# Optimization experiments

Hardware: AMD Instinct MI355X
Metric: run time of the kernel (lower is better)

The kernel has to match this reference:

```python
import jax, jax.numpy as jnp
import numpy as np

N, D, DP, H, S = 768, 384, 128, 8, 32
EPS = 1e-5  # haiku LayerNorm default eps


def _ln(x):
    # hk.LayerNorm([-1], create_scale=False, create_offset=False)
    mu = jnp.mean(x, axis=-1, keepdims=True)
    var = jnp.var(x, axis=-1, keepdims=True)
    return (x - mu) * jax.lax.rsqrt(var + EPS)


def setup_inputs() -> dict:
    key = jax.random.key(0)
    ks = jax.random.split(key, 12)
    local = jax.random.normal(ks[0], (N, D), dtype=jnp.float32)
    pair = jax.random.normal(ks[1], (N, N, DP), dtype=jnp.float32)
    mask = jnp.ones((N,), dtype=bool)
    sc = 0.02
    Wq = jax.random.normal(ks[2], (D, H * S), jnp.float32) * sc
    bq = jnp.zeros((H * S,), jnp.float32)
    Wk = jax.random.normal(ks[3], (D, H * S), jnp.float32) * sc
    bk = jnp.zeros((H * S,), jnp.float32)
    Wv = jax.random.normal(ks[4], (D, H * S), jnp.float32) * sc
    bv = jnp.zeros((H * S,), jnp.float32)
    Wpb = jax.random.normal(ks[5], (DP, H), jnp.float32) * sc   # pair -> attn bias, no bias term
    Wpv = jax.random.normal(ks[6], (DP, S), jnp.float32) * sc   # pair -> pair value, no bias term
    Wo = jax.random.normal(ks[7], (2 * H * S, D), jnp.float32) * sc  # zeros-init in original; random for testing
    return dict(local=local, pair=pair, mask=mask, Wq=Wq, bq=bq, Wk=Wk, bk=bk,
                Wv=Wv, bv=bv, Wpb=Wpb, Wpv=Wpv, Wo=Wo)


def reference(local, pair, mask, Wq, bq, Wk, bk, Wv, bv, Wpb, Wpv, Wo):
    n = local.shape[0]
    local_n = _ln(local)                       # [N, D]
    pair_n = _ln(pair)                         # [N, N, DP]

    q = _ln((local_n @ Wq + bq).reshape(n, H, S)) * (1.0 / jnp.sqrt(S + 1e-6))
    k = _ln((local_n @ Wk + bk).reshape(n, H, S))
    v = (local_n @ Wv + bv).reshape(n, H, S)

    pair_mask = mask[:, None] & mask[None, :]  # [N, N]
    attn = jnp.einsum('iha,jha->ijh', q, k)    # [N, N, H]
    attn = attn + jnp.einsum('ijd,dh->ijh', pair_n, Wpb)
    attn = jnp.where(pair_mask[..., None], attn, -1e9)
    attn = jax.nn.softmax(attn, axis=1)
    attn = jnp.where(pair_mask[..., None], attn, 0.0)

    out = jnp.einsum('ijh,jha->iha', attn, v).reshape(n, H * S)
    out_pair = jnp.einsum('ijd,da->ija', pair_n, Wpv)           # [N, N, S]
    out_pair = jnp.einsum('ijh,ija->iha', attn, out_pair).reshape(n, H * S)
    out = jnp.concatenate((out, out_pair), axis=-1)             # [N, 2*H*S]
    return out @ Wo                                             # [N, D]
```

## Files before the change

kernel.cpp:

```cpp
#include <hip/hip_runtime.h>

#define Nn 768
#define Dd 384
#define DPp 128
#define Hh 8
#define Ss 32

typedef short bf16x8 __attribute__((ext_vector_type(8)));
typedef float f32x4 __attribute__((ext_vector_type(4)));

__device__ __forceinline__ unsigned short f2bf(float f) {
  unsigned int u = __float_as_uint(f);
  u += 0x7fffu + ((u >> 16) & 1u);
  return (unsigned short)(u >> 16);
}
__device__ __forceinline__ float bf2f(unsigned short b) {
  return __uint_as_float(((unsigned int)b) << 16);
}

__global__ void k_prep(const float* __restrict__ Wpb, const float* __restrict__ Wpv,
                       const float* __restrict__ Wo,
                       unsigned short* __restrict__ wt, unsigned short* __restrict__ wot) {
  if (blockIdx.x < 12) {
    int idx = blockIdx.x * 512 + threadIdx.x;
    int o = idx >> 7, d = idx & 127;
    float v = 0.f;
    if (o < 8)       v = Wpb[d * 8 + o];
    else if (o < 40) v = Wpv[d * 32 + (o - 8)];
    wt[idx] = f2bf(v);
  } else {
    int n = blockIdx.x - 12;
    int k = threadIdx.x;
    wot[n * 512 + k] = f2bf(Wo[k * 384 + n]);
  }
}

__global__ __launch_bounds__(256)
void k_qkv(const float* __restrict__ local,
           const float* __restrict__ Wq, const float* __restrict__ bq,
           const float* __restrict__ Wk, const float* __restrict__ bk,
           const float* __restrict__ Wv, const float* __restrict__ bv,
           float* __restrict__ qw, float* __restrict__ kw, float* __restrict__ vw,
           unsigned short* __restrict__ vt, unsigned short* __restrict__ kt) {
  const int t = threadIdx.x;
  const int i0 = blockIdx.x * 4;
  __shared__ float xn[4][384];
  __shared__ float red[4][4][2];

  float a0[4], a1[4];
#pragma unroll
  for (int r = 0; r < 4; ++r) {
    const float* xr = local + (size_t)(i0 + r) * 384;
    a0[r] = xr[t];
    a1[r] = (t < 128) ? xr[256 + t] : 0.f;
    float s = a0[r] + a1[r];
    float s2 = a0[r] * a0[r] + a1[r] * a1[r];
#pragma unroll
    for (int m = 1; m < 64; m <<= 1) { s += __shfl_xor(s, m); s2 += __shfl_xor(s2, m); }
    if ((t & 63) == 0) { red[r][t >> 6][0] = s; red[r][t >> 6][1] = s2; }
  }
  __syncthreads();
#pragma unroll
  for (int r = 0; r < 4; ++r) {
    float s  = red[r][0][0] + red[r][1][0] + red[r][2][0] + red[r][3][0];
    float s2 = red[r][0][1] + red[r][1][1] + red[r][2][1] + red[r][3][1];
    float mu = s * (1.f / 384.f);
    float rr = rsqrtf(s2 * (1.f / 384.f) - mu * mu + 1e-5f);
    xn[r][t] = (a0[r] - mu) * rr;
    if (t < 128) xn[r][256 + t] = (a1[r] - mu) * rr;
  }
  __syncthreads();

  float accq[4], acck[4], accv[4];
  const float bqv = bq[t], bkv = bk[t], bvv = bv[t];
#pragma unroll
  for (int r = 0; r < 4; ++r) { accq[r] = bqv; acck[r] = bkv; accv[r] = bvv; }

  for (int dq = 0; dq < 96; ++dq) {
    float4 xv[4];
#pragma unroll
    for (int r = 0; r < 4; ++r) xv[r] = ((const float4*)xn[r])[dq];
#pragma unroll
    for (int e = 0; e < 4; ++e) {
      const int d = dq * 4 + e;
      const float wqv = Wq[d * 256 + t];
      const float wkv = Wk[d * 256 + t];
      const float wvv = Wv[d * 256 + t];
#pragma unroll
      for (int r = 0; r < 4; ++r) {
        float xe = (e == 0) ? xv[r].x : (e == 1) ? xv[r].y : (e == 2) ? xv[r].z : xv[r].w;
        accq[r] += xe * wqv; acck[r] += xe * wkv; accv[r] += xe * wvv;
      }
    }
  }

#pragma unroll
  for (int r = 0; r < 4; ++r) {
    float qs = accq[r], qs2 = accq[r] * accq[r];
    float ks = acck[r], ks2 = acck[r] * acck[r];
#pragma unroll
    for (int m = 1; m < 32; m <<= 1) {
      qs += __shfl_xor(qs, m); qs2 += __shfl_xor(qs2, m);
      ks += __shfl_xor(ks, m); ks2 += __shfl_xor(ks2, m);
    }
    float qmu = qs * (1.f / 32.f);
    float qr = rsqrtf(qs2 * (1.f / 32.f) - qmu * qmu + 1e-5f);
    float kmu = ks * (1.f / 32.f);
    float kr = rsqrtf(ks2 * (1.f / 32.f) - kmu * kmu + 1e-5f);
    size_t o = (size_t)(i0 + r) * 256 + t;
    float qv = (accq[r] - qmu) * qr * 0.17677669f;
    float kv = (acck[r] - kmu) * kr;
    qw[o] = qv;
    kw[o] = kv;
    vw[o] = accv[r];
    kt[o] = f2bf(kv);
    vt[(size_t)t * 768 + (i0 + r)] = f2bf(accv[r]);
  }
}

__global__ __launch_bounds__(256)
void k_pairA(const float* __restrict__ pair, const unsigned short* __restrict__ wt,
             unsigned short* __restrict__ biasb, unsigned short* __restrict__ pvg) {
  const int b = blockIdx.x;
  const int i = b / 12, jt = b % 12;
  const int j0 = jt * 64;
  const int tid = threadIdx.x;
  const int lane = tid & 63, w = tid >> 6;

  __shared__ unsigned short A_s[64 * 136];
  __shared__ unsigned short Wt_s[48 * 136];
  __shared__ float2 mur_s[64];

  for (int idx = tid; idx < 1536; idx += 256) {
    int row = idx >> 5, c = idx & 31;
    *(uint2*)(Wt_s + row * 136 + c * 4) = ((const uint2*)wt)[idx];
  }

  const float4* src = (const float4*)(pair + ((size_t)i * 768 + j0) * 128);
  float4 x[8];
#pragma unroll
  for (int u = 0; u < 8; ++u) x[u] = src[u * 256 + tid];

  const int half = lane >> 5;
#pragma unroll
  for (int u = 0; u < 8; ++u) {
    float4 v = x[u];
    float sm = v.x + v.y + v.z + v.w;
    float s2 = v.x * v.x + v.y * v.y + v.z * v.z + v.w * v.w;
    sm += __shfl_xor(sm, 1);  s2 += __shfl_xor(s2, 1);
    sm += __shfl_xor(sm, 2);  s2 += __shfl_xor(s2, 2);
    sm += __shfl_xor(sm, 4);  s2 += __shfl_xor(s2, 4);
    sm += __shfl_xor(sm, 8);  s2 += __shfl_xor(s2, 8);
    sm += __shfl_xor(sm, 16); s2 += __shfl_xor(s2, 16);
    if ((lane & 31) == 0) {
      float mu = sm * (1.f / 128.f);
      float rr = rsqrtf(s2 * (1.f / 128.f) - mu * mu + 1e-5f);
      mur_s[u * 8 + w * 2 + half] = make_float2(mu, rr);
    }
  }
  __syncthreads();

#pragma unroll
  for (int u = 0; u < 8; ++u) {
    int row = u * 8 + (tid >> 5);
    int c4 = tid & 31;
    float2 mr = mur_s[row];
    float4 v = x[u];
    unsigned int lo = ((unsigned int)f2bf((v.y - mr.x) * mr.y) << 16) | f2bf((v.x - mr.x) * mr.y);
    unsigned int hi = ((unsigned int)f2bf((v.w - mr.x) * mr.y) << 16) | f2bf((v.z - mr.x) * mr.y);
    *(uint2*)(A_s + row * 136 + c4 * 4) = make_uint2(lo, hi);
  }
  __syncthreads();

  const int col = lane & 15, q4 = lane >> 4;
  f32x4 acc0 = {0.f, 0.f, 0.f, 0.f}, acc1 = acc0, acc2 = acc0;
#pragma unroll
  for (int kk = 0; kk < 4; ++kk) {
    bf16x8 af = *(const bf16x8*)(A_s + (w * 16 + col) * 136 + kk * 32 + q4 * 8);
    bf16x8 b0 = *(const bf16x8*)(Wt_s + (col)      * 136 + kk * 32 + q4 * 8);
    bf16x8 b1 = *(const bf16x8*)(Wt_s + (16 + col) * 136 + kk * 32 + q4 * 8);
    bf16x8 b2 = *(const bf16x8*)(Wt_s + (32 + col) * 136 + kk * 32 + q4 * 8);
    acc0 = __builtin_amdgcn_mfma_f32_16x16x32_bf16(af, b0, acc0, 0, 0, 0);
    acc1 = __builtin_amdgcn_mfma_f32_16x16x32_bf16(af, b1, acc1, 0, 0, 0);
    acc2 = __builtin_amdgcn_mfma_f32_16x16x32_bf16(af, b2, acc2, 0, 0, 0);
  }
  __syncthreads();

  unsigned short* pv_st = A_s;
  unsigned short* b_st  = A_s + 2112;
  const int jl = w * 16 + q4 * 4;
#pragma unroll
  for (int reg = 0; reg < 4; ++reg) {
    int j = jl + reg;
    pv_st[j * 33 + (col + 8)] = f2bf(acc1[reg]);
    if (col < 8) {
      b_st[j * 9 + col] = f2bf(acc0[reg]);
      pv_st[j * 33 + (col + 24)] = f2bf(acc2[reg]);
    } else {
      pv_st[j * 33 + (col - 8)] = f2bf(acc0[reg]);
    }
  }
  __syncthreads();

  {
    const int a = tid >> 3, jc = tid & 7;
    unsigned short buf[8];
#pragma unroll
    for (int r = 0; r < 8; ++r) buf[r] = pv_st[(jc * 8 + r) * 33 + a];
    *(uint4*)(pvg + ((size_t)i * 32 + a) * 768 + j0 + jc * 8) = *(uint4*)buf;
  }
  if (tid < 64) {
    const int h = tid >> 3, jc = tid & 7;
    unsigned short buf[8];
#pragma unroll
    for (int r = 0; r < 8; ++r) buf[r] = b_st[(jc * 8 + r) * 9 + h];
    *(uint4*)(biasb + ((size_t)i * 8 + h) * 768 + j0 + jc * 8) = *(uint4*)buf;
  }
}

__device__ __forceinline__ float dot8(uint4 r, float4 qa, float4 qb) {
  return bf2f((unsigned short)(r.x & 0xffffu)) * qa.x + bf2f((unsigned short)(r.x >> 16)) * qa.y
       + bf2f((unsigned short)(r.y & 0xffffu)) * qa.z + bf2f((unsigned short)(r.y >> 16)) * qa.w
       + bf2f((unsigned short)(r.z & 0xffffu)) * qb.x + bf2f((unsigned short)(r.z >> 16)) * qb.y
       + bf2f((unsigned short)(r.w & 0xffffu)) * qb.z + bf2f((unsigned short)(r.w >> 16)) * qb.w;
}

__global__ __launch_bounds__(512)
void k_soft(const unsigned short* __restrict__ biasb,
            const float* __restrict__ qw, const unsigned short* __restrict__ kt,
            unsigned short* __restrict__ pbuf) {
  const int i = blockIdx.x;
  const int tid = threadIdx.x;
  const int lane = tid & 63;
  const int wv = tid >> 6;

  __shared__ float logit_s[8 * 776];
  __shared__ float q_s[256];

  const unsigned short* bsrc = biasb + (size_t)i * 6144;
  for (int idx = tid; idx < 1536; idx += 512) {
    uint2 w = ((const uint2*)bsrc)[idx];
    int h = idx / 192, c = (idx % 192) * 4;
    float* dst = logit_s + h * 776 + c;
    dst[0] = bf2f((unsigned short)(w.x & 0xffffu));
    dst[1] = bf2f((unsigned short)(w.x >> 16));
    dst[2] = bf2f((unsigned short)(w.y & 0xffffu));
    dst[3] = bf2f((unsigned short)(w.y >> 16));
  }
  if (tid < 256) q_s[tid] = qw[(size_t)i * 256 + tid];
  __syncthreads();

  for (int rep = 0; rep < 12; ++rep) {
    int idx = rep * 512 + tid;
    int j = idx >> 3, h = idx & 7;
    const unsigned short* kp = kt + (size_t)j * 256 + h * 32;
    const float4* qp = (const float4*)(q_s + h * 32);
    uint4 r0 = *(const uint4*)(kp);
    uint4 r1 = *(const uint4*)(kp + 8);
    uint4 r2 = *(const uint4*)(kp + 16);
    uint4 r3 = *(const uint4*)(kp + 24);
    float d = dot8(r0, qp[0], qp[1]) + dot8(r1, qp[2], qp[3])
            + dot8(r2, qp[4], qp[5]) + dot8(r3, qp[6], qp[7]);
    logit_s[h * 776 + j] += d;
  }
  __syncthreads();

  {
    const int h = wv;
    float* lr = logit_s + h * 776;
    float mx = -3.0e38f;
#pragma unroll
    for (int rr = 0; rr < 12; ++rr) mx = fmaxf(mx, lr[rr * 64 + lane]);
#pragma unroll
    for (int m = 1; m < 64; m <<= 1) mx = fmaxf(mx, __shfl_xor(mx, m));
    float e[12];
    float sum = 0.f;
#pragma unroll
    for (int rr = 0; rr < 12; ++rr) {
      e[rr] = __expf(lr[rr * 64 + lane] - mx);
      sum += e[rr];
    }
#pragma unroll
    for (int m = 1; m < 64; m <<= 1) sum += __shfl_xor(sum, m);
    const float rinv = 1.f / sum;
    unsigned short* dst = pbuf + ((size_t)h * 768 + i) * 768;
#pragma unroll
    for (int rr = 0; rr < 12; ++rr)
      dst[rr * 64 + lane] = f2bf(e[rr] * rinv);
  }
}

__global__ __launch_bounds__(128)
void k_mm(const unsigned short* __restrict__ pbuf, const unsigned short* __restrict__ vt,
          const unsigned short* __restrict__ pvg, unsigned short* __restrict__ concat_bf) {
  const int b = blockIdx.x;
  const int tid = threadIdx.x;
  const int nt = tid >> 6, lane = tid & 63;
  const int col = lane & 15, q4 = lane >> 4;

  if (b < 384) {
    const int h = b / 48, it = b % 48;
    const int i0 = it * 16;
    const unsigned short* ap = pbuf + ((size_t)h * 768 + i0 + col) * 768 + q4 * 8;
    const unsigned short* bp = vt + ((size_t)h * 32 + nt * 16 + col) * 768 + q4 * 8;
    f32x4 acc = {0.f, 0.f, 0.f, 0.f};
#pragma unroll
    for (int kk = 0; kk < 24; ++kk) {
      bf16x8 a = *(const bf16x8*)(ap + kk * 32);
      bf16x8 bb = *(const bf16x8*)(bp + kk * 32);
      acc = __builtin_amdgcn_mfma_f32_16x16x32_bf16(a, bb, acc, 0, 0, 0);
    }
#pragma unroll
    for (int reg = 0; reg < 4; ++reg) {
      int i = i0 + q4 * 4 + reg;
      concat_bf[(size_t)i * 512 + h * 32 + nt * 16 + col] = f2bf(acc[reg]);
    }
  } else {
    const int i = b - 384;
    const int hrow = (col < 8) ? col : 7;
    const unsigned short* ap = pbuf + ((size_t)hrow * 768 + i) * 768 + q4 * 8;
    const unsigned short* bp = pvg + ((size_t)i * 32 + nt * 16 + col) * 768 + q4 * 8;
    f32x4 acc = {0.f, 0.f, 0.f, 0.f};
#pragma unroll
    for (int kk = 0; kk < 24; ++kk) {
      bf16x8 a = *(const bf16x8*)(ap + kk * 32);
      bf16x8 bb = *(const bf16x8*)(bp + kk * 32);
      acc = __builtin_amdgcn_mfma_f32_16x16x32_bf16(a, bb, acc, 0, 0, 0);
    }
    if (q4 < 2) {
#pragma unroll
      for (int reg = 0; reg < 4; ++reg) {
        int hh = q4 * 4 + reg;
        concat_bf[(size_t)i * 512 + 256 + hh * 32 + nt * 16 + col] = f2bf(acc[reg]);
      }
    }
  }
}

__global__ __launch_bounds__(256)
void k_out2(const unsigned short* __restrict__ concat_bf, const unsigned short* __restrict__ wot,
            float* __restrict__ out) {
  const int b = blockIdx.x;
  const int i0 = (b / 6) * 16;
  const int tid = threadIdx.x;
  const int nt = tid >> 6, lane = tid & 63;
  const int n0 = (b % 6) * 64 + nt * 16;
  const int col = lane & 15, q4 = lane >> 4;

  const unsigned short* ap = concat_bf + (size_t)(i0 + col) * 512 + q4 * 8;
  const unsigned short* bp = wot + (size_t)(n0 + col) * 512 + q4 * 8;
  f32x4 acc = {0.f, 0.f, 0.f, 0.f};
#pragma unroll
  for (int kk = 0; kk < 16; ++kk) {
    bf16x8 a = *(const bf16x8*)(ap + kk * 32);
    bf16x8 bb = *(const bf16x8*)(bp + kk * 32);
    acc = __builtin_amdgcn_mfma_f32_16x16x32_bf16(a, bb, acc, 0, 0, 0);
  }
#pragma unroll
  for (int reg = 0; reg < 4; ++reg) {
    int i = i0 + q4 * 4 + reg;
    out[(size_t)i * 384 + n0 + col] = acc[reg];
  }
}

__global__ __launch_bounds__(512)
void k_pair_fused(const float* __restrict__ pair,
                  const float* __restrict__ qw, const float* __restrict__ kw,
                  const float* __restrict__ vw, const unsigned short* __restrict__ wt,
                  float* __restrict__ concat) {
  const int i = blockIdx.x;
  const int tid = threadIdx.x;
  const int lane = tid & 63;
  const int wv = tid >> 6;

  __shared__ float xt[64 * 132];
  __shared__ unsigned short A_s[64 * 136];
  __shared__ unsigned short Wt_s[48 * 136];
  __shared__ unsigned short pv_s[32 * 772];
  __shared__ float logit_s[768 * 9];
  __shared__ float2 mur_s[64];
  __shared__ float q_s[256];
  __shared__ float rinv_s[8];

  for (int idx = tid; idx < 48 * 128; idx += 512)
    Wt_s[(idx >> 7) * 136 + (idx & 127)] = wt[idx];
  if (tid < 256) q_s[tid] = qw[(size_t)i * 256 + tid];

  for (int tt = 0; tt < 12; ++tt) {
    const int j0 = tt * 64;
    const float4* src = (const float4*)(pair + ((size_t)i * 768 + j0) * 128);
    __syncthreads();
#pragma unroll
    for (int r = 0; r < 4; ++r) {
      int qi = r * 512 + tid;
      float4 x = src[qi];
      ((float4*)(xt + (qi >> 5) * 132))[qi & 31] = x;
    }
    __syncthreads();
    if (tid < 256) {
      int j = tid >> 2, s = tid & 3;
      const float4* b = (const float4*)(xt + j * 132 + s * 32);
      float sm = 0.f, s2 = 0.f;
#pragma unroll
      for (int u = 0; u < 8; ++u) {
        float4 x = b[u];
        sm += x.x + x.y + x.z + x.w;
        s2 += x.x * x.x + x.y * x.y + x.z * x.z + x.w * x.w;
      }
      sm += __shfl_xor(sm, 1); s2 += __shfl_xor(s2, 1);
      sm += __shfl_xor(sm, 2); s2 += __shfl_xor(s2, 2);
      if (s == 0) {
        float mu = sm * (1.f / 128.f);
        float rr = rsqrtf(s2 * (1.f / 128.f) - mu * mu + 1e-5f);
        mur_s[j] = make_float2(mu, rr);
      }
    }
    __syncthreads();
#pragma unroll
    for (int r = 0; r < 4; ++r) {
      int qi = r * 512 + tid;
      int jj = qi >> 5, ql = qi & 31;
      float4 x = ((const float4*)(xt + jj * 132))[ql];
      float2 mr = mur_s[jj];
      unsigned int b01 = ((unsigned int)f2bf((x.y - mr.x) * mr.y) << 16) | f2bf((x.x - mr.x) * mr.y);
      unsigned int b23 = ((unsigned int)f2bf((x.w - mr.x) * mr.y) << 16) | f2bf((x.z - mr.x) * mr.y);
      *(uint2*)(A_s + jj * 136 + ql * 4) = make_uint2(b01, b23);
    }
    __syncthreads();
    if (wv < 4) {
      const int col = lane & 15, q4 = lane >> 4;
      f32x4 acc0 = {0.f, 0.f, 0.f, 0.f}, acc1 = acc0, acc2 = acc0;
#pragma unroll
      for (int kk = 0; kk < 4; ++kk) {
        bf16x8 af = *(const bf16x8*)(A_s + (wv * 16 + col) * 136 + kk * 32 + q4 * 8);
        bf16x8 b0 = *(const bf16x8*)(Wt_s + (col)      * 136 + kk * 32 + q4 * 8);
        bf16x8 b1 = *(const bf16x8*)(Wt_s + (16 + col) * 136 + kk * 32 + q4 * 8);
        bf16x8 b2 = *(const bf16x8*)(Wt_s + (32 + col) * 136 + kk * 32 + q4 * 8);
        acc0 = __builtin_amdgcn_mfma_f32_16x16x32_bf16(af, b0, acc0, 0, 0, 0);
        acc1 = __builtin_amdgcn_mfma_f32_16x16x32_bf16(af, b1, acc1, 0, 0, 0);
        acc2 = __builtin_amdgcn_mfma_f32_16x16x32_bf16(af, b2, acc2, 0, 0, 0);
      }
      const int jb = j0 + wv * 16 + q4 * 4;
#pragma unroll
      for (int reg = 0; reg < 4; ++reg) {
        int j = jb + reg;
        if (col < 8) logit_s[j * 9 + col] = acc0[reg];
        else         pv_s[(col - 8) * 772 + j] = f2bf(acc0[reg]);
        pv_s[(col + 8) * 772 + j] = f2bf(acc1[reg]);
        if (col < 8) pv_s[(col + 24) * 772 + j] = f2bf(acc2[reg]);
      }
    }
  }
  __syncthreads();

  for (int rep = 0; rep < 12; ++rep) {
    int idx = rep * 512 + tid;
    int j = idx >> 3, h = idx & 7;
    const float4* kp = (const float4*)(kw + ((size_t)j * 8 + h) * 32);
    const float4* qp = (const float4*)(q_s + h * 32);
    float d = 0.f;
#pragma unroll
    for (int u = 0; u < 8; ++u) {
      float4 a = qp[u], b = kp[u];
      d += a.x * b.x + a.y * b.y + a.z * b.z + a.w * b.w;
    }
    logit_s[j * 9 + h] += d;
  }
  __syncthreads();

  float* pT = xt;
  {
    const int h = wv;
    float mx = -3.0e38f;
#pragma unroll
    for (int rr = 0; rr < 12; ++rr) mx = fmaxf(mx, logit_s[(rr * 64 + lane) * 9 + h]);
#pragma unroll
    for (int m = 1; m < 64; m <<= 1) mx = fmaxf(mx, __shfl_xor(mx, m));
    float sum = 0.f;
#pragma unroll
    for (int rr = 0; rr < 12; ++rr) {
      int j = rr * 64 + lane;
      float e = __expf(logit_s[j * 9 + h] - mx);
      pT[h * 768 + j] = e;
      sum += e;
    }
#pragma unroll
    for (int m = 1; m < 64; m <<= 1) sum += __shfl_xor(sum, m);
    if (lane == 0) rinv_s[h] = 1.f / sum;
  }
  __syncthreads();

  float acc = 0.f;
  if (tid < 256) {
    const int h = tid >> 5, a = tid & 31;
    const float* vcol = vw + h * 32 + a;
    const float4* p4p = (const float4*)(pT + h * 768);
#pragma unroll 4
    for (int j4 = 0; j4 < 192; ++j4) {
      float4 p = p4p[j4];
      const float* vb = vcol + (size_t)(j4 * 4) * 256;
      acc += p.x * vb[0] + p.y * vb[256] + p.z * vb[512] + p.w * vb[768];
    }
    acc *= rinv_s[h];
  } else {
    const int u = tid - 256;
    const int h = u >> 5, a = u & 31;
    const float4* p4p = (const float4*)(pT + h * 768);
    const unsigned short* pvrow = pv_s + a * 772;
#pragma unroll 4
    for (int j4 = 0; j4 < 192; ++j4) {
      float4 p = p4p[j4];
      uint2 raw = *(const uint2*)(pvrow + j4 * 4);
      acc += p.x * bf2f((unsigned short)(raw.x & 0xffffu))
           + p.y * bf2f((unsigned short)(raw.x >> 16))
           + p.z * bf2f((unsigned short)(raw.y & 0xffffu))
           + p.w * bf2f((unsigned short)(raw.y >> 16));
    }
    acc *= rinv_s[h];
  }
  concat[(size_t)i * 512 + tid] = acc;
}

__global__ __launch_bounds__(384)
void k_out_f32(const float* __restrict__ concat, const float* __restrict__ Wo,
               float* __restrict__ out) {
  __shared__ float A_s[4 * 512];
  const int d = threadIdx.x;
  const int r0 = blockIdx.x * 4;
  const float4* src = (const float4*)(concat + (size_t)r0 * 512);
  for (int idx = d; idx < 512; idx += 384) ((float4*)A_s)[idx] = src[idx];
  __syncthreads();

  float acc[4] = {0.f, 0.f, 0.f, 0.f};
#pragma unroll 4
  for (int c4 = 0; c4 < 128; ++c4) {
    float w0 = Wo[(c4 * 4 + 0) * 384 + d];
    float w1 = Wo[(c4 * 4 + 1) * 384 + d];
    float w2 = Wo[(c4 * 4 + 2) * 384 + d];
    float w3 = Wo[(c4 * 4 + 3) * 384 + d];
#pragma unroll
    for (int r = 0; r < 4; ++r) {
      float4 a = ((const float4*)(A_s + r * 512))[c4];
      acc[r] += a.x * w0 + a.y * w1 + a.z * w2 + a.w * w3;
    }
  }
#pragma unroll
  for (int r = 0; r < 4; ++r) out[(size_t)(r0 + r) * 384 + d] = acc[r];
}

extern "C" void kernel_launch(void* const* d_in, const int* in_sizes, int n_in,
                              void* d_out, int out_size, void* d_ws, size_t ws_size,
                              hipStream_t stream) {
  (void)in_sizes; (void)n_in; (void)out_size;
  const float* local = (const float*)d_in[0];
  const float* pair  = (const float*)d_in[1];
  const float* Wq  = (const float*)d_in[3];
  const float* bq  = (const float*)d_in[4];
  const float* Wk  = (const float*)d_in[5];
  const float* bk  = (const float*)d_in[6];
  const float* Wv  = (const float*)d_in[7];
  const float* bv  = (const float*)d_in[8];
  const float* Wpb = (const float*)d_in[9];
  const float* Wpv = (const float*)d_in[10];
  const float* Wo  = (const float*)d_in[11];

  float* ws = (float*)d_ws;
  float* qw = ws;
  float* kw = qw + 196608;
  float* vw = kw + 196608;
  float* concat = vw + 196608;
  unsigned short* wt   = (unsigned short*)(concat + 393216);
  unsigned short* vt   = wt + 6144;
  unsigned short* kt   = vt + 196608;
  unsigned short* wot  = kt + 196608;
  unsigned short* biasb = wot + 196608;
  unsigned short* pvg  = biasb + 4718592;
  unsigned short* pbuf = pvg + 18874368;
  unsigned short* concat_bf = pbuf + 4718592;

  hipLaunchKernelGGL(k_prep, dim3(396), dim3(512), 0, stream, Wpb, Wpv, Wo, wt, wot);
  hipLaunchKernelGGL(k_qkv, dim3(192), dim3(256), 0, stream,
                     local, Wq, bq, Wk, bk, Wv, bv, qw, kw, vw, vt, kt);
  if (ws_size >= 62533632ull) {
    hipLaunchKernelGGL(k_pairA, dim3(9216), dim3(256), 0, stream, pair, wt, biasb, pvg);
    hipLaunchKernelGGL(k_soft, dim3(768), dim3(512), 0, stream, biasb, qw, kt, pbuf);
    hipLaunchKernelGGL(k_mm, dim3(1152), dim3(128), 0, stream, pbuf, vt, pvg, concat_bf);
    hipLaunchKernelGGL(k_out2, dim3(288), dim3(256), 0, stream, concat_bf, wot, (float*)d_out);
  } else {
    hipLaunchKernelGGL(k_pair_fused, dim3(768), dim3(512), 0, stream,
                       pair, qw, kw, vw, wt, concat);
    hipLaunchKernelGGL(k_out_f32, dim3(192), dim3(384), 0, stream, concat, Wo, (float*)d_out);
  }
}
```

Before: 537.7 us.

## Fuse QK logits into pair kernel and merge prep with QKV kernel

The q·k dot products move out of the softmax kernel into the pair-projection kernel. There they are added in fp32 to the pair bias before a single bf16 store, so the softmax kernel only reads finished logits. The weight-prep and QKV projection kernels are also merged into one launch with block-range dispatch, which removes one kernel launch. The cost is extra register and LDS pressure and extra K/q loads in the heavily launched pair kernel, though the biasb intermediate no longer needs to be rounded to bf16 before q·k is added.

```diff
diff --git a/kernel.cpp b/kernel.cpp
--- a/kernel.cpp
+++ b/kernel.cpp
@@ -17,33 +17,42 @@
 __device__ __forceinline__ float bf2f(unsigned short b) {
   return __uint_as_float(((unsigned int)b) << 16);
 }
-
-__global__ void k_prep(const float* __restrict__ Wpb, const float* __restrict__ Wpv,
-                       const float* __restrict__ Wo,
-                       unsigned short* __restrict__ wt, unsigned short* __restrict__ wot) {
-  if (blockIdx.x < 12) {
-    int idx = blockIdx.x * 512 + threadIdx.x;
+__device__ __forceinline__ float dot8(uint4 r, float4 qa, float4 qb) {
+  return bf2f((unsigned short)(r.x & 0xffffu)) * qa.x + bf2f((unsigned short)(r.x >> 16)) * qa.y
+       + bf2f((unsigned short)(r.y & 0xffffu)) * qa.z + bf2f((unsigned short)(r.y >> 16)) * qa.w
+       + bf2f((unsigned short)(r.z & 0xffffu)) * qb.x + bf2f((unsigned short)(r.z >> 16)) * qb.y
+       + bf2f((unsigned short)(r.w & 0xffffu)) * qb.z + bf2f((unsigned short)(r.w >> 16)) * qb.w;
+}
+
+__global__ __launch_bounds__(256)
+void k_front(const float* __restrict__ local,
+             const float* __restrict__ Wq, const float* __restrict__ bq,
+             const float* __restrict__ Wk, const float* __restrict__ bk,
+             const float* __restrict__ Wv, const float* __restrict__ bv,
+             const float* __restrict__ Wpb, const float* __restrict__ Wpv,
+             const float* __restrict__ Wo,
+             float* __restrict__ qw, float* __restrict__ kw, float* __restrict__ vw,
+             unsigned short* __restrict__ vt, unsigned short* __restrict__ kt,
+             unsigned short* __restrict__ wt, unsigned short* __restrict__ wot) {
+  const int b = blockIdx.x;
+  const int t = threadIdx.x;
+  if (b >= 216) {
+    int idx = (b - 216) * 256 + t;
+    int n = idx >> 9, k = idx & 511;
+    wot[idx] = f2bf(Wo[k * 384 + n]);
+    return;
+  }
+  if (b >= 192) {
+    int idx = (b - 192) * 256 + t;
     int o = idx >> 7, d = idx & 127;
     float v = 0.f;
     if (o < 8)       v = Wpb[d * 8 + o];
     else if (o < 40) v = Wpv[d * 32 + (o - 8)];
     wt[idx] = f2bf(v);
-  } else {
-    int n = blockIdx.x - 12;
-    int k = threadIdx.x;
-    wot[n * 512 + k] = f2bf(Wo[k * 384 + n]);
-  }
-}
-
-__global__ __launch_bounds__(256)
-void k_qkv(const float* __restrict__ local,
-           const float* __restrict__ Wq, const float* __restrict__ bq,
-           const float* __restrict__ Wk, const float* __restrict__ bk,
-           const float* __restrict__ Wv, const float* __restrict__ bv,
-           float* __restrict__ qw, float* __restrict__ kw, float* __restrict__ vw,
-           unsigned short* __restrict__ vt, unsigned short* __restrict__ kt) {
-  const int t = threadIdx.x;
-  const int i0 = blockIdx.x * 4;
+    return;
+  }
+
+  const int i0 = b * 4;
   __shared__ float xn[4][384];
   __shared__ float red[4][4][2];
 
@@ -120,7 +129,8 @@
 
 __global__ __launch_bounds__(256)
 void k_pairA(const float* __restrict__ pair, const unsigned short* __restrict__ wt,
-             unsigned short* __restrict__ biasb, unsigned short* __restrict__ pvg) {
+             const float* __restrict__ qw, const unsigned short* __restrict__ kt,
+             unsigned short* __restrict__ logitb, unsigned short* __restrict__ pvg) {
   const int b = blockIdx.x;
   const int i = b / 12, jt = b % 12;
   const int j0 = jt * 64;
@@ -130,16 +140,19 @@
   __shared__ unsigned short A_s[64 * 136];
   __shared__ unsigned short Wt_s[48 * 136];
   __shared__ float2 mur_s[64];
+  __shared__ float q_s[256];
+
+  const float4* src = (const float4*)(pair + ((size_t)i * 768 + j0) * 128);
+  float4 x[8];
+#pragma unroll
+  for (int u = 0; u < 8; ++u) x[u] = src[u * 256 + tid];
+
+  q_s[tid] = qw[(size_t)i * 256 + tid];
 
   for (int idx = tid; idx < 1536; idx += 256) {
     int row = idx >> 5, c = idx & 31;
     *(uint2*)(Wt_s + row * 136 + c * 4) = ((const uint2*)wt)[idx];
   }
-
-  const float4* src = (const float4*)(pair + ((size_t)i * 768 + j0) * 128);
-  float4 x[8];
-#pragma unroll
-  for (int u = 0; u < 8; ++u) x[u] = src[u * 256 + tid];
 
   const int half = lane >> 5;
 #pragma unroll
@@ -170,6 +183,15 @@
     unsigned int hi = ((unsigned int)f2bf((v.w - mr.x) * mr.y) << 16) | f2bf((v.z - mr.x) * mr.y);
     *(uint2*)(A_s + row * 136 + c4 * 4) = make_uint2(lo, hi);
   }
+
+  const int qj = tid >> 3, qh = tid & 7;
+  uint4 k0[4], k1[4];
+  {
+    const unsigned short* kp0 = kt + (size_t)(j0 + qj) * 256 + qh * 32;
+    const unsigned short* kp1 = kp0 + 32 * 256;
+#pragma unroll
+    for (int u = 0; u < 4; ++u) { k0[u] = *(const uint4*)(kp0 + u * 8); k1[u] = *(const uint4*)(kp1 + u * 8); }
+  }
   __syncthreads();
 
   const int col = lane & 15, q4 = lane >> 4;
@@ -184,17 +206,26 @@
     acc1 = __builtin_amdgcn_mfma_f32_16x16x32_bf16(af, b1, acc1, 0, 0, 0);
     acc2 = __builtin_amdgcn_mfma_f32_16x16x32_bf16(af, b2, acc2, 0, 0, 0);
   }
+
+  float d0, d1;
+  {
+    const float4* qp = (const float4*)(q_s + qh * 32);
+    float4 qa = qp[0], qb = qp[1], qc = qp[2], qd = qp[3];
+    float4 qe = qp[4], qf = qp[5], qg = qp[6], qqh = qp[7];
+    d0 = dot8(k0[0], qa, qb) + dot8(k0[1], qc, qd) + dot8(k0[2], qe, qf) + dot8(k0[3], qg, qqh);
+    d1 = dot8(k1[0], qa, qb) + dot8(k1[1], qc, qd) + dot8(k1[2], qe, qf) + dot8(k1[3], qg, qqh);
+  }
   __syncthreads();
 
   unsigned short* pv_st = A_s;
-  unsigned short* b_st  = A_s + 2112;
+  float* b_st = (float*)(A_s + 2112);
   const int jl = w * 16 + q4 * 4;
 #pragma unroll
   for (int reg = 0; reg < 4; ++reg) {
     int j = jl + reg;
     pv_st[j * 33 + (col + 8)] = f2bf(acc1[reg]);
     if (col < 8) {
-      b_st[j * 9 + col] = f2bf(acc0[reg]);
+      b_st[j * 9 + col] = acc0[reg];
       pv_st[j * 33 + (col + 24)] = f2bf(acc2[reg]);
     } else {
       pv_st[j * 33 + (col - 8)] = f2bf(acc0[reg]);
@@ -209,35 +240,29 @@
     for (int r = 0; r < 8; ++r) buf[r] = pv_st[(jc * 8 + r) * 33 + a];
     *(uint4*)(pvg + ((size_t)i * 32 + a) * 768 + j0 + jc * 8) = *(uint4*)buf;
   }
+  b_st[qj * 9 + qh] += d0;
+  b_st[(qj + 32) * 9 + qh] += d1;
+  __syncthreads();
+
   if (tid < 64) {
     const int h = tid >> 3, jc = tid & 7;
     unsigned short buf[8];
 #pragma unroll
-    for (int r = 0; r < 8; ++r) buf[r] = b_st[(jc * 8 + r) * 9 + h];
-    *(uint4*)(biasb + ((size_t)i * 8 + h) * 768 + j0 + jc * 8) = *(uint4*)buf;
-  }
-}
-
-__device__ __forceinline__ float dot8(uint4 r, float4 qa, float4 qb) {
-  return bf2f((unsigned short)(r.x & 0xffffu)) * qa.x + bf2f((unsigned short)(r.x >> 16)) * qa.y
-       + bf2f((unsigned short)(r.y & 0xffffu)) * qa.z + bf2f((unsigned short)(r.y >> 16)) * qa.w
-       + bf2f((unsigned short)(r.z & 0xffffu)) * qb.x + bf2f((unsigned short)(r.z >> 16)) * qb.y
-       + bf2f((unsigned short)(r.w & 0xffffu)) * qb.z + bf2f((unsigned short)(r.w >> 16)) * qb.w;
+    for (int r = 0; r < 8; ++r) buf[r] = f2bf(b_st[(jc * 8 + r) * 9 + h]);
+    *(uint4*)(logitb + ((size_t)i * 8 + h) * 768 + j0 + jc * 8) = *(uint4*)buf;
+  }
 }
 
 __global__ __launch_bounds__(512)
-void k_soft(const unsigned short* __restrict__ biasb,
-            const float* __restrict__ qw, const unsigned short* __restrict__ kt,
-            unsigned short* __restrict__ pbuf) {
+void k_soft(const unsigned short* __restrict__ logitb, unsigned short* __restrict__ pbuf) {
   const int i = blockIdx.x;
   const int tid = threadIdx.x;
   const int lane = tid & 63;
   const int wv = tid >> 6;
 
   __shared__ float logit_s[8 * 776];
-  __shared__ float q_s[256];
-
-  const unsigned short* bsrc = biasb + (size_t)i * 6144;
+
+  const unsigned short* bsrc = logitb + (size_t)i * 6144;
   for (int idx = tid; idx < 1536; idx += 512) {
     uint2 w = ((const uint2*)bsrc)[idx];
     int h = idx / 192, c = (idx % 192) * 4;
@@ -246,22 +271,6 @@
     dst[1] = bf2f((unsigned short)(w.x >> 16));
     dst[2] = bf2f((unsigned short)(w.y & 0xffffu));
     dst[3] = bf2f((unsigned short)(w.y >> 16));
-  }
-  if (tid < 256) q_s[tid] = qw[(size_t)i * 256 + tid];
-  __syncthreads();
-
-  for (int rep = 0; rep < 12; ++rep) {
-    int idx = rep * 512 + tid;
-    int j = idx >> 3, h = idx & 7;
-    const unsigned short* kp = kt + (size_t)j * 256 + h * 32;
-    const float4* qp = (const float4*)(q_s + h * 32);
-    uint4 r0 = *(const uint4*)(kp);
-    uint4 r1 = *(const uint4*)(kp + 8);
-    uint4 r2 = *(const uint4*)(kp + 16);
-    uint4 r3 = *(const uint4*)(kp + 24);
-    float d = dot8(r0, qp[0], qp[1]) + dot8(r1, qp[2], qp[3])
-            + dot8(r2, qp[4], qp[5]) + dot8(r3, qp[6], qp[7]);
-    logit_s[h * 776 + j] += d;
   }
   __syncthreads();
 
@@ -573,17 +582,17 @@
   unsigned short* vt   = wt + 6144;
   unsigned short* kt   = vt + 196608;
   unsigned short* wot  = kt + 196608;
-  unsigned short* biasb = wot + 196608;
-  unsigned short* pvg  = biasb + 4718592;
+  unsigned short* logitb = wot + 196608;
+  unsigned short* pvg  = logitb + 4718592;
   unsigned short* pbuf = pvg + 18874368;
   unsigned short* concat_bf = pbuf + 4718592;
 
-  hipLaunchKernelGGL(k_prep, dim3(396), dim3(512), 0, stream, Wpb, Wpv, Wo, wt, wot);
-  hipLaunchKernelGGL(k_qkv, dim3(192), dim3(256), 0, stream,
-                     local, Wq, bq, Wk, bk, Wv, bv, qw, kw, vw, vt, kt);
+  hipLaunchKernelGGL(k_front, dim3(984), dim3(256), 0, stream,
+                     local, Wq, bq, Wk, bk, Wv, bv, Wpb, Wpv, Wo,
+                     qw, kw, vw, vt, kt, wt, wot);
   if (ws_size >= 62533632ull) {
-    hipLaunchKernelGGL(k_pairA, dim3(9216), dim3(256), 0, stream, pair, wt, biasb, pvg);
-    hipLaunchKernelGGL(k_soft, dim3(768), dim3(512), 0, stream, biasb, qw, kt, pbuf);
+    hipLaunchKernelGGL(k_pairA, dim3(9216), dim3(256), 0, stream, pair, wt, qw, kt, logitb, pvg);
+    hipLaunchKernelGGL(k_soft, dim3(768), dim3(512), 0, stream, logitb, pbuf);
     hipLaunchKernelGGL(k_mm, dim3(1152), dim3(128), 0, stream, pbuf, vt, pvg, concat_bf);
     hipLaunchKernelGGL(k_out2, dim3(288), dim3(256), 0, stream, concat_bf, wot, (float*)d_out);
   } else {
```

Result: no change. 542.8 us (+0.9%).
